# Optimization experiments

Hardware: AMD Instinct MI355X
Metric: run time of the kernel (lower is better)

## Reference

```python
import jax, jax.numpy as jnp
import numpy as np

N, F_IN, F_OUT, H = 4096, 128, 64, 8
NEG_SLOPE = 0.2

def leaky_relu(x):
    return jnp.where(x >= 0, x, NEG_SLOPE * x)

def setup_inputs() -> dict:
    key = jax.random.key(0)
    k = jax.random.split(key, 6)
    x = jax.random.normal(k[0], (N, F_IN), dtype=jnp.float32)
    conn = jax.random.uniform(k[1], (N, N)) < 0.1
    conn = conn | jnp.eye(N, dtype=bool)
    topology = jnp.where(conn, 0.0, -1e9).astype(jnp.float32)
    proj = jax.random.normal(k[2], (H, F_IN, F_OUT), dtype=jnp.float32) * (1.0 / np.sqrt(F_IN))
    score_src = jax.random.normal(k[3], (H, F_OUT), dtype=jnp.float32) * (1.0 / np.sqrt(F_OUT))
    score_dst = jax.random.normal(k[4], (H, F_OUT), dtype=jnp.float32) * (1.0 / np.sqrt(F_OUT))
    skip_w = jax.random.normal(k[5], (H * F_OUT, F_IN), dtype=jnp.float32) * (1.0 / np.sqrt(F_IN))
    return {"x": x, "topology": topology, "proj": proj,
            "score_src": score_src, "score_dst": score_dst, "skip_w": skip_w}

def reference(x, topology, proj, score_src, score_dst, skip_w):
    # dropout is identity at inference time
    # projected node features: [H, N, F_OUT]
    h = jnp.einsum('ni,hio->hno', x, proj)
    # additive attention scores (GAT): [H, N, 1] + [H, 1, N] -> [H, N, N]
    s_src = jnp.einsum('hno,ho->hn', h, score_src)
    s_dst = jnp.einsum('hno,ho->hn', h, score_dst)
    scores = leaky_relu(s_src[:, :, None] + s_dst[:, None, :])
    attn = jax.nn.softmax(scores + topology[None, :, :], axis=-1)  # [H, N, N]
    # aggregate neighbors, then transpose heads to [N, H, F_OUT]
    out = jnp.einsum('hij,hjo->iho', attn, h)
    # skip connection (F_OUT != F_IN -> projected skip)
    out = out + (x @ skip_w.T).reshape(N, H, F_OUT)
    # mean over heads (concat_heads=False), then LeakyReLU activation
    out = leaky_relu(jnp.mean(out, axis=1))  # [N, F_OUT]
    return out
```

## Files before the change

### kernel.cpp

```cpp
#include <hip/hip_runtime.h>
#include <hip/hip_bf16.h>

#define NN 4096
#define FIN 128
#define FOUT 64
#define NH 8
#define KS 4
#define QT 32

typedef float f32x4 __attribute__((ext_vector_type(4)));
typedef _Float16 f16x8 __attribute__((ext_vector_type(8)));
typedef _Float16 h2 __attribute__((ext_vector_type(2)));
typedef unsigned long long u64;

static __device__ __forceinline__ h2 as_h2(unsigned u) { return __builtin_bit_cast(h2, u); }
static __device__ __forceinline__ unsigned as_u32(h2 v) { return __builtin_bit_cast(unsigned, v); }

__global__ __launch_bounds__(256) void maskwc_kernel(
    const float* __restrict__ topo, u64* __restrict__ mb,
    const float* __restrict__ proj, const float* __restrict__ score_src,
    const float* __restrict__ score_dst, const float* __restrict__ skip_w,
    float* __restrict__ Wc) {
    const int tid = threadIdx.x;
    if (blockIdx.x < 2048) {
        const int w = blockIdx.x * 4 + (tid >> 6);
        const int lane = tid & 63;
        size_t base = (size_t)w * 32;
#pragma unroll 4
        for (int it = 0; it < 32; ++it) {
            size_t u = base + it;
            float t = topo[u * 64 + lane];
            u64 b = __ballot(t > -0.5e9f);
            if (lane == 0) mb[u] = b;
        }
        return;
    }
    int idx = (blockIdx.x - 2048) * 256 + tid;
    if (idx >= FIN * 80) return;
    int i = idx / 80, c = idx % 80;
    float v = 0.f;
    if (c < 16) {
        int h = c & 7;
        const float* w = (c < 8 ? score_src : score_dst) + h * FOUT;
        const float* p = proj + (size_t)h * FIN * FOUT + (size_t)i * FOUT;
        for (int f = 0; f < FOUT; ++f) v += p[f] * w[f];
    } else {
        int f = c - 16;
        for (int h = 0; h < NH; ++h) v += skip_w[(size_t)(h * FOUT + f) * FIN + i];
        v *= 0.125f;
    }
    Wc[i * 80 + c] = v;
}

__global__ __launch_bounds__(256) void scores_kernel(
    const float* __restrict__ x, const float* __restrict__ Wc,
    float* __restrict__ skipm, _Float16* __restrict__ Eh, _Float16* __restrict__ Fh,
    unsigned* __restrict__ Cc, _Float16* __restrict__ xb) {
    __shared__ float wcs[FIN][80];
    __shared__ float xs[16][FIN + 5];
    const int n0 = blockIdx.x * 16;
    const int tid = threadIdx.x;
    for (int i = tid; i < FIN * 80 / 4; i += 256)
        ((float4*)&wcs[0][0])[i] = ((const float4*)Wc)[i];
    const float4* xsrc = (const float4*)(x + (size_t)n0 * FIN);
    for (int i = tid; i < 16 * FIN / 4; i += 256) {
        int r = i >> 5, c4 = i & 31;
        *(float4*)&xs[r][c4 * 4] = xsrc[i];
    }
    __syncthreads();
    const int r = tid & 15;
    const int g = tid >> 4;
    float acc[4];
    float sa = 0.f;
#pragma unroll
    for (int j = 0; j < 4; ++j) acc[j] = 0.f;
#pragma unroll 4
    for (int i = 0; i < FIN; ++i) {
        float xv = xs[r][i];
        float4 p = *(float4*)&wcs[i][16 + g * 4];
        float qv = wcs[i][g];
        acc[0] += xv * p.x; acc[1] += xv * p.y; acc[2] += xv * p.z; acc[3] += xv * p.w;
        sa += xv * qv;
    }
    int n = n0 + r;
#pragma unroll
    for (int j = 0; j < 4; ++j) skipm[(size_t)n * FOUT + g * 4 + j] = acc[j];
    if (g < 8) {
        _Float16 c1 = (_Float16)(expf(sa) * 0.125f);
        _Float16 c2 = (_Float16)(expf(0.2f * sa) * 0.125f);
        unsigned short u1 = __builtin_bit_cast(unsigned short, c1);
        unsigned short u2 = __builtin_bit_cast(unsigned short, c2);
        Cc[(size_t)g * NN + n] = ((unsigned)u2 << 16) | (unsigned)u1;
    } else {
        int h = g - 8;
        Eh[(size_t)h * NN + n] = (_Float16)expf(sa);
        Fh[(size_t)h * NN + n] = (_Float16)expf(0.2f * sa);
    }
    {
        int row = tid >> 4, col0 = (tid & 15) * 8;
        const float* src = &xs[row][col0];
        f16x8 b0;
#pragma unroll
        for (int j = 0; j < 8; ++j) b0[j] = (_Float16)src[j];
        *(f16x8*)(xb + (size_t)(n0 + row) * FIN + col0) = b0;
    }
}

__global__ __launch_bounds__(256) void vt_kernel(
    const float* __restrict__ proj, const _Float16* __restrict__ xb,
    _Float16* __restrict__ Vt) {
    __shared__ _Float16 pT[FOUT][FIN + 8];
    const int tid = threadIdx.x;
    const int h = blockIdx.x >> 6;
    const int ng = blockIdx.x & 63;
    for (int idx = tid; idx < FIN * FOUT; idx += 256) {
        int i = idx >> 6, f = idx & 63;
        pT[f][i] = (_Float16)proj[(size_t)h * FIN * FOUT + idx];
    }
    __syncthreads();
    const int wave = tid >> 6, lane = tid & 63, q = lane >> 4, li = lane & 15;
    const int nb = ng * 64 + wave * 16;
    f32x4 acc[4];
#pragma unroll
    for (int n = 0; n < 4; ++n) acc[n] = (f32x4){0.f, 0.f, 0.f, 0.f};
#pragma unroll
    for (int kt = 0; kt < 4; ++kt) {
        f16x8 bfrag = *(const f16x8*)(xb + (size_t)(nb + li) * FIN + kt * 32 + q * 8);
#pragma unroll
        for (int ft = 0; ft < 4; ++ft) {
            f16x8 afrag = *(const f16x8*)&pT[ft * 16 + li][kt * 32 + q * 8];
            acc[ft] = __builtin_amdgcn_mfma_f32_16x16x32_f16(afrag, bfrag, acc[ft], 0, 0, 0);
        }
    }
#pragma unroll
    for (int ft = 0; ft < 4; ++ft)
#pragma unroll
        for (int reg = 0; reg < 4; ++reg)
            Vt[((size_t)h * FOUT + ft * 16 + q * 4 + reg) * NN + nb + li] = (_Float16)acc[ft][reg];
}

__attribute__((amdgpu_waves_per_eu(4)))
__global__ __launch_bounds__(256) void attn_kernel(
    const u64* __restrict__ maskbits, const _Float16* __restrict__ Vtg,
    const _Float16* __restrict__ Ehg, const _Float16* __restrict__ Fhg,
    const unsigned* __restrict__ Ccg,
    __hip_bfloat16* __restrict__ accP, float* __restrict__ rsP) {
    __shared__ u64 maskS[QT][17];
    __shared__ char vA[4][4096];
    __shared__ char vB[4][4096];
    const int tid = threadIdx.x;
    const int w = tid >> 6;
    const int lane = tid & 63, q = lane >> 4, li = lane & 15;
    const int qt = blockIdx.x >> 3, ks = (blockIdx.x >> 1) & 3, hb = blockIdx.x & 1;
    const int h = hb * 4 + w;
    const int row0 = qt * QT;
    const int kb0 = ks * 1024;

    const int r_ = lane >> 2;
    const int sg = ((lane & 3) - (r_ >> 1)) & 3;
    const size_t laneoff = (size_t)r_ * NN + sg * 8;
    const int rdoff = li * 64 + ((q + (li >> 1)) & 3) * 16;

    const _Float16* vb = Vtg + (size_t)h * (FOUT * NN) + kb0;
    const _Float16* Ehq = Ehg + (size_t)h * NN + kb0 + q * 8;
    const _Float16* Fhq = Fhg + (size_t)h * NN + kb0 + q * 8;

#define DMA_TILE(DST, KT) do {                                                     \
    _Pragma("unroll")                                                              \
    for (int c = 0; c < 4; ++c) {                                                  \
        const _Float16* g_ = vb + (size_t)c * (16 * NN) + (KT) * 32 + laneoff;     \
        __builtin_amdgcn_global_load_lds(                                          \
            (const __attribute__((address_space(1))) void*)g_,                     \
            (__attribute__((address_space(3))) void*)&DST[w][c * 1024], 16, 0, 0); \
    }                                                                              \
} while (0)

    DMA_TILE(vA, 0);
    {
        int i0 = tid, i1 = tid + 256;
        maskS[i0 >> 4][i0 & 15] = maskbits[(size_t)(row0 + (i0 >> 4)) * 64 + ks * 16 + (i0 & 15)];
        maskS[i1 >> 4][i1 & 15] = maskbits[(size_t)(row0 + (i1 >> 4)) * 64 + ks * 16 + (i1 & 15)];
    }
    __syncthreads();

    h2 c1h[2], c2h[2];
#pragma unroll
    for (int rt = 0; rt < 2; ++rt) {
        unsigned cw = Ccg[(size_t)h * NN + row0 + rt * 16 + li];
        c1h[rt] = as_h2((cw << 16) | (cw & 0xffffu));
        c2h[rt] = as_h2((cw >> 16) | (cw & 0xffff0000u));
    }
    f16x8 ones;
#pragma unroll
    for (int j = 0; j < 8; ++j) ones[j] = (_Float16)1.0f;

    f32x4 acc[2][4];
    f32x4 rsacc[2];
#pragma unroll
    for (int rt = 0; rt < 2; ++rt) {
#pragma unroll
        for (int n = 0; n < 4; ++n) acc[rt][n] = (f32x4){0.f, 0.f, 0.f, 0.f};
        rsacc[rt] = (f32x4){0.f, 0.f, 0.f, 0.f};
    }

#define CHUNK_BODY(SRC, DSTN, KT) do {                                                        \
    uint4 ea_ = *(const uint4*)(Ehq + (KT) * 32);                                             \
    uint4 fa_ = *(const uint4*)(Fhq + (KT) * 32);                                             \
    asm volatile("" ::: "memory");                          \
    DMA_TILE(DSTN, ((KT) + 1) & 31);                                                          \
    asm volatile("s_waitcnt vmcnt(4)" ::: "memory");                                          \
    f16x8 vf_[4];                                                                             \
    _Pragma("unroll")                                                                         \
    for (int n = 0; n < 4; ++n)                                                               \
        vf_[n] = *(const f16x8*)&SRC[w][n * 1024 + rdoff];                                    \
    unsigned ew_[4] = {ea_.x, ea_.y, ea_.z, ea_.w};                                           \
    unsigned fw_[4] = {fa_.x, fa_.y, fa_.z, fa_.w};                                           \
    _Pragma("unroll")                                                                         \
    for (int rt = 0; rt < 2; ++rt) {                                                          \
        u64 mw_ = maskS[rt * 16 + li][(KT) >> 1];                                             \
        unsigned mm_ = (unsigned)(mw_ >> (((KT) & 1) * 32 + q * 8)) & 0xffu;                  \
        unsigned blo_ = ((mm_ & 0xFu) * 0x204081u) & 0x01010101u;                             \
        unsigned bhi_ = ((mm_ >> 4) * 0x204081u) & 0x01010101u;                               \
        blo_ *= 0xFFu; bhi_ *= 0xFFu;                                                         \
        unsigned mk_[4] = {__builtin_amdgcn_perm(0u, blo_, 0x01010000u),                      \
                           __builtin_amdgcn_perm(0u, blo_, 0x03030202u),                      \
                           __builtin_amdgcn_perm(0u, bhi_, 0x01010000u),                      \
                           __builtin_amdgcn_perm(0u, bhi_, 0x03030202u)};                     \
        union { f16x8 v; unsigned u[4]; } pf_;                                                \
        _Pragma("unroll")                                                                     \
        for (int j2 = 0; j2 < 4; ++j2) {                                                      \
            h2 t_ = c1h[rt] * as_h2(ew_[j2]);                                                 \
            h2 u_ = c2h[rt] * as_h2(fw_[j2]);                                                 \
            h2 p_ = __builtin_elementwise_max(t_, u_);                                        \
            pf_.u[j2] = as_u32(p_) & mk_[j2];                                                 \
        }                                                                                     \
        rsacc[rt] = __builtin_amdgcn_mfma_f32_16x16x32_f16(pf_.v, ones, rsacc[rt], 0, 0, 0);  \
        _Pragma("unroll")                                                                     \
        for (int n = 0; n < 4; ++n)                                                           \
            acc[rt][n] = __builtin_amdgcn_mfma_f32_16x16x32_f16(pf_.v, vf_[n], acc[rt][n],    \
                                                                0, 0, 0);                     \
    }                                                                                         \
} while (0)

#pragma unroll 1
    for (int kt = 0; kt < 32; kt += 2) {
        CHUNK_BODY(vA, vB, kt);
        CHUNK_BODY(vB, vA, kt + 1);
    }
#undef CHUNK_BODY
#undef DMA_TILE

#pragma unroll
    for (int rt = 0; rt < 2; ++rt) {
        if (li == 0) {
#pragma unroll
            for (int reg = 0; reg < 4; ++reg)
                rsP[(size_t)(ks * NH + h) * NN + row0 + rt * 16 + q * 4 + reg] = rsacc[rt][reg];
        }
        __hip_bfloat16* ap = accP + ((size_t)(ks * NH + h) * NN + row0 + rt * 16) * 64;
#pragma unroll
        for (int n = 0; n < 4; ++n)
#pragma unroll
            for (int reg = 0; reg < 4; ++reg)
                ap[(q * 4 + reg) * 64 + n * 16 + li] = __float2bfloat16(acc[rt][n][reg]);
    }
}

__global__ __launch_bounds__(256) void combine_kernel(
    const __hip_bfloat16* __restrict__ accP, const float* __restrict__ rsP,
    float* __restrict__ out) {
    int idx = blockIdx.x * 256 + threadIdx.x;
    int row = idx >> 6, f = idx & 63;
    float s = 0.f;
#pragma unroll 1
    for (int h = 0; h < NH; ++h) {
        float a = 0.f, r = 0.f;
#pragma unroll
        for (int k = 0; k < KS; ++k) {
            a += __bfloat162float(accP[((size_t)(k * NH + h) * NN + row) * 64 + f]);
            r += rsP[(size_t)(k * NH + h) * NN + row];
        }
        s += a / r;
    }
    float v = s * 0.125f + out[idx];
    out[idx] = fmaxf(v, 0.2f * v);
}

extern "C" void kernel_launch(void* const* d_in, const int* in_sizes, int n_in,
                              void* d_out, int out_size, void* d_ws, size_t ws_size,
                              hipStream_t stream) {
    (void)in_sizes; (void)n_in; (void)out_size; (void)ws_size;
    const float* x         = (const float*)d_in[0];
    const float* topology  = (const float*)d_in[1];
    const float* proj      = (const float*)d_in[2];
    const float* score_src = (const float*)d_in[3];
    const float* score_dst = (const float*)d_in[4];
    const float* skip_w    = (const float*)d_in[5];
    float* out = (float*)d_out;

    char* ws = (char*)d_ws;
    _Float16* xb   = (_Float16*)ws;
    _Float16* Vt   = (_Float16*)(ws + 1048576);
    _Float16* Eh   = (_Float16*)(ws + 5242880);
    _Float16* Fh   = (_Float16*)(ws + 5308416);
    unsigned* Cc   = (unsigned*)(ws + 5373952);
    float* Wc      = (float*)(ws + 5505024);
    u64* maskbits  = (u64*)(ws + 5545984);
    float* rsP     = (float*)(ws + 7643136);
    __hip_bfloat16* accP = (__hip_bfloat16*)(ws + 8167424);
    float* skipm = out;

    maskwc_kernel<<<2088, 256, 0, stream>>>(topology, maskbits, proj, score_src,
                                            score_dst, skip_w, Wc);
    scores_kernel<<<256, 256, 0, stream>>>(x, Wc, skipm, Eh, Fh, Cc, xb);
    vt_kernel<<<512, 256, 0, stream>>>(proj, xb, Vt);
    attn_kernel<<<1024, 256, 0, stream>>>(maskbits, Vt, Eh, Fh, Cc, accP, rsP);
    combine_kernel<<<1024, 256, 0, stream>>>(accP, rsP, out);
}
```

Measured before the change: 179.2 us.

## Load V fragments directly from global into registers with double-buffered prefetch

Removes the LDS staging of V tiles via global_load_lds and instead loads each lane's V fragments straight from global memory into registers, prefetching two chunks ahead in a register double buffer. Mask words are also prefetched one iteration ahead, and the bit-expand multiply is replaced with shifts and ORs. This drops the LDS round trip, the explicit vmcnt waits and the shared buffers, which may improve occupancy. The cost is more VGPR pressure and direct global loads whose per-lane access pattern is less coalesced. The loop also reads V, E and F past the last chunk, at offsets up to ks*1024+1120 into the slice.

```diff
diff --git a/kernel.cpp b/kernel.cpp
--- a/kernel.cpp
+++ b/kernel.cpp
@@ -146,8 +146,6 @@
     const unsigned* __restrict__ Ccg,
     __hip_bfloat16* __restrict__ accP, float* __restrict__ rsP) {
     __shared__ u64 maskS[QT][17];
-    __shared__ char vA[4][4096];
-    __shared__ char vB[4][4096];
     const int tid = threadIdx.x;
     const int w = tid >> 6;
     const int lane = tid & 63, q = lane >> 4, li = lane & 15;
@@ -156,31 +154,28 @@
     const int row0 = qt * QT;
     const int kb0 = ks * 1024;
 
-    const int r_ = lane >> 2;
-    const int sg = ((lane & 3) - (r_ >> 1)) & 3;
-    const size_t laneoff = (size_t)r_ * NN + sg * 8;
-    const int rdoff = li * 64 + ((q + (li >> 1)) & 3) * 16;
-
-    const _Float16* vb = Vtg + (size_t)h * (FOUT * NN) + kb0;
-    const _Float16* Ehq = Ehg + (size_t)h * NN + kb0 + q * 8;
-    const _Float16* Fhq = Fhg + (size_t)h * NN + kb0 + q * 8;
-
-#define DMA_TILE(DST, KT) do {                                                     \
-    _Pragma("unroll")                                                              \
-    for (int c = 0; c < 4; ++c) {                                                  \
-        const _Float16* g_ = vb + (size_t)c * (16 * NN) + (KT) * 32 + laneoff;     \
-        __builtin_amdgcn_global_load_lds(                                          \
-            (const __attribute__((address_space(1))) void*)g_,                     \
-            (__attribute__((address_space(3))) void*)&DST[w][c * 1024], 16, 0, 0); \
-    }                                                                              \
-} while (0)
-
-    DMA_TILE(vA, 0);
+    const _Float16* vb0 = Vtg + ((size_t)h * FOUT + li) * NN + kb0 + q * 8;
+    const _Float16* vb1 = vb0 + 16 * NN;
+    const _Float16* vb2 = vb0 + 32 * NN;
+    const _Float16* vb3 = vb0 + 48 * NN;
+    const _Float16* ehp = Ehg + (size_t)h * NN + kb0 + q * 8;
+    const _Float16* fhp = Fhg + (size_t)h * NN + kb0 + q * 8;
+
     {
         int i0 = tid, i1 = tid + 256;
         maskS[i0 >> 4][i0 & 15] = maskbits[(size_t)(row0 + (i0 >> 4)) * 64 + ks * 16 + (i0 & 15)];
         maskS[i1 >> 4][i1 & 15] = maskbits[(size_t)(row0 + (i1 >> 4)) * 64 + ks * 16 + (i1 & 15)];
     }
+
+    f16x8 vfA[4], vfB[4];
+    uint4 eA, fA, eB, fB;
+    vfA[0] = *(const f16x8*)(vb0);       vfA[1] = *(const f16x8*)(vb1);
+    vfA[2] = *(const f16x8*)(vb2);       vfA[3] = *(const f16x8*)(vb3);
+    eA = *(const uint4*)(ehp);           fA = *(const uint4*)(fhp);
+    vfB[0] = *(const f16x8*)(vb0 + 32);  vfB[1] = *(const f16x8*)(vb1 + 32);
+    vfB[2] = *(const f16x8*)(vb2 + 32);  vfB[3] = *(const f16x8*)(vb3 + 32);
+    eB = *(const uint4*)(ehp + 32);      fB = *(const uint4*)(fhp + 32);
+
     __syncthreads();
 
     h2 c1h[2], c2h[2];
@@ -203,25 +198,21 @@
         rsacc[rt] = (f32x4){0.f, 0.f, 0.f, 0.f};
     }
 
-#define CHUNK_BODY(SRC, DSTN, KT) do {                                                        \
-    uint4 ea_ = *(const uint4*)(Ehq + (KT) * 32);                                             \
-    uint4 fa_ = *(const uint4*)(Fhq + (KT) * 32);                                             \
-    asm volatile("" ::: "memory");                          \
-    DMA_TILE(DSTN, ((KT) + 1) & 31);                                                          \
-    asm volatile("s_waitcnt vmcnt(4)" ::: "memory");                                          \
-    f16x8 vf_[4];                                                                             \
-    _Pragma("unroll")                                                                         \
-    for (int n = 0; n < 4; ++n)                                                               \
-        vf_[n] = *(const f16x8*)&SRC[w][n * 1024 + rdoff];                                    \
-    unsigned ew_[4] = {ea_.x, ea_.y, ea_.z, ea_.w};                                           \
-    unsigned fw_[4] = {fa_.x, fa_.y, fa_.z, fa_.w};                                           \
+    const u64* mp = &maskS[li][0];
+    u64 mw0 = mp[0], mw1 = mp[272];
+
+#define CHUNK_BODY(VF, EE, FF, PAR, PRE) do {                                                 \
+    unsigned ew_[4] = {EE.x, EE.y, EE.z, EE.w};                                               \
+    unsigned fw_[4] = {FF.x, FF.y, FF.z, FF.w};                                               \
     _Pragma("unroll")                                                                         \
     for (int rt = 0; rt < 2; ++rt) {                                                          \
-        u64 mw_ = maskS[rt * 16 + li][(KT) >> 1];                                             \
-        unsigned mm_ = (unsigned)(mw_ >> (((KT) & 1) * 32 + q * 8)) & 0xffu;                  \
-        unsigned blo_ = ((mm_ & 0xFu) * 0x204081u) & 0x01010101u;                             \
-        unsigned bhi_ = ((mm_ >> 4) * 0x204081u) & 0x01010101u;                               \
-        blo_ *= 0xFFu; bhi_ *= 0xFFu;                                                         \
+        u64 mw_ = rt ? mw1 : mw0;                                                             \
+        unsigned mm_ = (unsigned)(mw_ >> ((PAR) * 32 + q * 8)) & 0xffu;                       \
+        unsigned mlo_ = mm_ & 0xFu, mhi_ = mm_ >> 4;                                          \
+        unsigned blo_ = (mlo_ | (mlo_ << 7) | (mlo_ << 14) | (mlo_ << 21)) & 0x01010101u;     \
+        unsigned bhi_ = (mhi_ | (mhi_ << 7) | (mhi_ << 14) | (mhi_ << 21)) & 0x01010101u;     \
+        blo_ = (blo_ << 8) - blo_;                                                            \
+        bhi_ = (bhi_ << 8) - bhi_;                                                            \
         unsigned mk_[4] = {__builtin_amdgcn_perm(0u, blo_, 0x01010000u),                      \
                            __builtin_amdgcn_perm(0u, blo_, 0x03030202u),                      \
                            __builtin_amdgcn_perm(0u, bhi_, 0x01010000u),                      \
@@ -237,18 +228,27 @@
         rsacc[rt] = __builtin_amdgcn_mfma_f32_16x16x32_f16(pf_.v, ones, rsacc[rt], 0, 0, 0);  \
         _Pragma("unroll")                                                                     \
         for (int n = 0; n < 4; ++n)                                                           \
-            acc[rt][n] = __builtin_amdgcn_mfma_f32_16x16x32_f16(pf_.v, vf_[n], acc[rt][n],    \
+            acc[rt][n] = __builtin_amdgcn_mfma_f32_16x16x32_f16(pf_.v, VF[n], acc[rt][n],     \
                                                                 0, 0, 0);                     \
     }                                                                                         \
+    VF[0] = *(const f16x8*)(vb0 + (PRE));                                                     \
+    VF[1] = *(const f16x8*)(vb1 + (PRE));                                                     \
+    VF[2] = *(const f16x8*)(vb2 + (PRE));                                                     \
+    VF[3] = *(const f16x8*)(vb3 + (PRE));                                                     \
+    EE = *(const uint4*)(ehp + (PRE));                                                        \
+    FF = *(const uint4*)(fhp + (PRE));                                                        \
 } while (0)
 
 #pragma unroll 1
-    for (int kt = 0; kt < 32; kt += 2) {
-        CHUNK_BODY(vA, vB, kt);
-        CHUNK_BODY(vB, vA, kt + 1);
+    for (int i = 0; i < 16; ++i) {
+        u64 mn0 = mp[1], mn1 = mp[273];
+        CHUNK_BODY(vfA, eA, fA, 0, 64);
+        CHUNK_BODY(vfB, eB, fB, 1, 96);
+        mw0 = mn0; mw1 = mn1; ++mp;
+        vb0 += 64; vb1 += 64; vb2 += 64; vb3 += 64;
+        ehp += 64; fhp += 64;
     }
 #undef CHUNK_BODY
-#undef DMA_TILE
 
 #pragma unroll
     for (int rt = 0; rt < 2; ++rt) {
```

Measured after the change: 213.4 us. 1.19x slower.

## Share V tiles across waves with one head per block and a 4-deep LDS ring

Applied to the files above, without the earlier changes.

Each block now handles a single head. Its four waves cover different 32-row query groups and cooperatively DMA one shared V tile into a 4-buffer LDS ring, with a block barrier at every chunk. The goal is to cut per-block V traffic from global memory and L2 by reusing each tile across four waves. E/F score loads are now software-prefetched in registers, mask words are preloaded from LDS, and the byte-mask expansion uses shifts instead of multiplies. In exchange there is a barrier per chunk, the last prefetches read past the key slice, and the mask stored in LDS grows.

```diff
diff --git a/kernel.cpp b/kernel.cpp
--- a/kernel.cpp
+++ b/kernel.cpp
@@ -6,7 +6,6 @@
 #define FOUT 64
 #define NH 8
 #define KS 4
-#define QT 32
 
 typedef float f32x4 __attribute__((ext_vector_type(4)));
 typedef _Float16 f16x8 __attribute__((ext_vector_type(8)));
@@ -145,43 +144,42 @@
     const _Float16* __restrict__ Ehg, const _Float16* __restrict__ Fhg,
     const unsigned* __restrict__ Ccg,
     __hip_bfloat16* __restrict__ accP, float* __restrict__ rsP) {
-    __shared__ u64 maskS[QT][17];
-    __shared__ char vA[4][4096];
-    __shared__ char vB[4][4096];
+    __shared__ u64 maskS[4][32][18];
+    __shared__ char vbuf[4][4096];
     const int tid = threadIdx.x;
     const int w = tid >> 6;
     const int lane = tid & 63, q = lane >> 4, li = lane & 15;
-    const int qt = blockIdx.x >> 3, ks = (blockIdx.x >> 1) & 3, hb = blockIdx.x & 1;
-    const int h = hb * 4 + w;
-    const int row0 = qt * QT;
+    const int qt = blockIdx.x >> 5;
+    const int ks = (blockIdx.x >> 3) & 3;
+    const int h  = blockIdx.x & 7;
+    const int row0 = qt * 128 + w * 32;
     const int kb0 = ks * 1024;
 
     const int r_ = lane >> 2;
     const int sg = ((lane & 3) - (r_ >> 1)) & 3;
-    const size_t laneoff = (size_t)r_ * NN + sg * 8;
+    const _Float16* gsrc = Vtg + ((size_t)h * FOUT + w * 16 + r_) * NN + kb0 + sg * 8;
     const int rdoff = li * 64 + ((q + (li >> 1)) & 3) * 16;
-
-    const _Float16* vb = Vtg + (size_t)h * (FOUT * NN) + kb0;
-    const _Float16* Ehq = Ehg + (size_t)h * NN + kb0 + q * 8;
-    const _Float16* Fhq = Fhg + (size_t)h * NN + kb0 + q * 8;
-
-#define DMA_TILE(DST, KT) do {                                                     \
-    _Pragma("unroll")                                                              \
-    for (int c = 0; c < 4; ++c) {                                                  \
-        const _Float16* g_ = vb + (size_t)c * (16 * NN) + (KT) * 32 + laneoff;     \
-        __builtin_amdgcn_global_load_lds(                                          \
-            (const __attribute__((address_space(1))) void*)g_,                     \
-            (__attribute__((address_space(3))) void*)&DST[w][c * 1024], 16, 0, 0); \
-    }                                                                              \
-} while (0)
-
-    DMA_TILE(vA, 0);
+    const _Float16* ehp = Ehg + (size_t)h * NN + kb0 + q * 8;
+    const _Float16* fhp = Fhg + (size_t)h * NN + kb0 + q * 8;
+
+#define DMA_TILE(B, OFF) \
+    __builtin_amdgcn_global_load_lds( \
+        (const __attribute__((address_space(1))) void*)(gsrc + (OFF)), \
+        (__attribute__((address_space(3))) void*)&vbuf[B][w * 1024], 16, 0, 0)
+
     {
-        int i0 = tid, i1 = tid + 256;
-        maskS[i0 >> 4][i0 & 15] = maskbits[(size_t)(row0 + (i0 >> 4)) * 64 + ks * 16 + (i0 & 15)];
-        maskS[i1 >> 4][i1 & 15] = maskbits[(size_t)(row0 + (i1 >> 4)) * 64 + ks * 16 + (i1 & 15)];
-    }
-    __syncthreads();
+#pragma unroll
+        for (int j = 0; j < 8; ++j) {
+            int t = lane + j * 64;
+            maskS[w][t >> 4][t & 15] =
+                maskbits[(size_t)(row0 + (t >> 4)) * 64 + ks * 16 + (t & 15)];
+        }
+    }
+    uint4 e0 = *(const uint4*)(ehp);
+    uint4 f0 = *(const uint4*)(fhp);
+    uint4 e1, f1;
+    DMA_TILE(0, 0);
+    DMA_TILE(1, 32);
 
     h2 c1h[2], c2h[2];
 #pragma unroll
@@ -190,6 +188,8 @@
         c1h[rt] = as_h2((cw << 16) | (cw & 0xffffu));
         c2h[rt] = as_h2((cw >> 16) | (cw & 0xffff0000u));
     }
+    __syncthreads();
+
     f16x8 ones;
 #pragma unroll
     for (int j = 0; j < 8; ++j) ones[j] = (_Float16)1.0f;
@@ -203,25 +203,33 @@
         rsacc[rt] = (f32x4){0.f, 0.f, 0.f, 0.f};
     }
 
-#define CHUNK_BODY(SRC, DSTN, KT) do {                                                        \
-    uint4 ea_ = *(const uint4*)(Ehq + (KT) * 32);                                             \
-    uint4 fa_ = *(const uint4*)(Fhq + (KT) * 32);                                             \
-    asm volatile("" ::: "memory");                          \
-    DMA_TILE(DSTN, ((KT) + 1) & 31);                                                          \
+    const u64* mp0 = &maskS[w][li][0];
+    const u64* mp1 = &maskS[w][16 + li][0];
+    u64 ma0 = mp0[0], ma1 = mp1[0];
+    u64 mb0 = mp0[1], mb1 = mp1[1];
+
+#define BODY(K2, EU, FU, EN, FN, MW0, MW1) do {                                               \
+    EN = *(const uint4*)(ehp + ((K2) + 1) * 32);                                              \
+    FN = *(const uint4*)(fhp + ((K2) + 1) * 32);                                              \
+    asm volatile("" ::: "memory");                        \
+    DMA_TILE(((K2) + 2) & 3, ((K2) + 2) * 32);                                                \
     asm volatile("s_waitcnt vmcnt(4)" ::: "memory");                                          \
+    __builtin_amdgcn_s_barrier();                                                             \
     f16x8 vf_[4];                                                                             \
     _Pragma("unroll")                                                                         \
     for (int n = 0; n < 4; ++n)                                                               \
-        vf_[n] = *(const f16x8*)&SRC[w][n * 1024 + rdoff];                                    \
-    unsigned ew_[4] = {ea_.x, ea_.y, ea_.z, ea_.w};                                           \
-    unsigned fw_[4] = {fa_.x, fa_.y, fa_.z, fa_.w};                                           \
+        vf_[n] = *(const f16x8*)&vbuf[K2][n * 1024 + rdoff];                                  \
+    unsigned ew_[4] = {EU.x, EU.y, EU.z, EU.w};                                               \
+    unsigned fw_[4] = {FU.x, FU.y, FU.z, FU.w};                                               \
     _Pragma("unroll")                                                                         \
     for (int rt = 0; rt < 2; ++rt) {                                                          \
-        u64 mw_ = maskS[rt * 16 + li][(KT) >> 1];                                             \
-        unsigned mm_ = (unsigned)(mw_ >> (((KT) & 1) * 32 + q * 8)) & 0xffu;                  \
-        unsigned blo_ = ((mm_ & 0xFu) * 0x204081u) & 0x01010101u;                             \
-        unsigned bhi_ = ((mm_ >> 4) * 0x204081u) & 0x01010101u;                               \
-        blo_ *= 0xFFu; bhi_ *= 0xFFu;                                                         \
+        u64 mw_ = rt ? (MW1) : (MW0);                                                         \
+        unsigned mm_ = (unsigned)(mw_ >> (((K2) & 1) * 32 + q * 8)) & 0xffu;                  \
+        unsigned mlo_ = mm_ & 0xFu, mhi_ = mm_ >> 4;                                          \
+        unsigned blo_ = (mlo_ | (mlo_ << 7) | (mlo_ << 14) | (mlo_ << 21)) & 0x01010101u;     \
+        unsigned bhi_ = (mhi_ | (mhi_ << 7) | (mhi_ << 14) | (mhi_ << 21)) & 0x01010101u;     \
+        blo_ = (blo_ << 8) - blo_;                                                            \
+        bhi_ = (bhi_ << 8) - bhi_;                                                            \
         unsigned mk_[4] = {__builtin_amdgcn_perm(0u, blo_, 0x01010000u),                      \
                            __builtin_amdgcn_perm(0u, blo_, 0x03030202u),                      \
                            __builtin_amdgcn_perm(0u, bhi_, 0x01010000u),                      \
@@ -243,12 +251,21 @@
 } while (0)
 
 #pragma unroll 1
-    for (int kt = 0; kt < 32; kt += 2) {
-        CHUNK_BODY(vA, vB, kt);
-        CHUNK_BODY(vB, vA, kt + 1);
-    }
-#undef CHUNK_BODY
+    for (int i = 0; i < 8; ++i) {
+        u64 na0 = mp0[2], na1 = mp1[2];
+        u64 nb0 = mp0[3], nb1 = mp1[3];
+        BODY(0, e0, f0, e1, f1, ma0, ma1);
+        BODY(1, e1, f1, e0, f0, ma0, ma1);
+        BODY(2, e0, f0, e1, f1, mb0, mb1);
+        BODY(3, e1, f1, e0, f0, mb0, mb1);
+        ma0 = na0; ma1 = na1; mb0 = nb0; mb1 = nb1;
+        mp0 += 2; mp1 += 2;
+        gsrc += 128; ehp += 128; fhp += 128;
+    }
+#undef BODY
 #undef DMA_TILE
+
+    asm volatile("s_waitcnt vmcnt(0)" ::: "memory");
 
 #pragma unroll
     for (int rt = 0; rt < 2; ++rt) {
```

New measurement: 171.9 us. 4.1% less time.
